# Performance work log

Measured on AMD Instinct MI355X. Metric: run time of the kernel, lower is better.

## Reference

```python
import jax, jax.numpy as jnp
import numpy as np

B, L, E, H, EXP = 2, 2048, 1024, 16, 4
D = E // H
EPS = 1e-5

def layernorm(x, g, b):
    mu = jnp.mean(x, axis=-1, keepdims=True)
    var = jnp.var(x, axis=-1, keepdims=True)
    return (x - mu) * jax.lax.rsqrt(var + EPS) * g + b

def setup_inputs() -> dict:
    key = jax.random.key(0)
    ks = jax.random.split(key, 12)
    s = 0.02
    return {
        "x": jax.random.normal(ks[0], (B, L, E), dtype=jnp.float32),
        "ln1_g": jnp.ones((E,), jnp.float32),
        "ln1_b": jnp.zeros((E,), jnp.float32),
        "W_qkv": jax.random.normal(ks[1], (E, 3 * E), dtype=jnp.float32) * s,
        "W_proj": jax.random.normal(ks[2], (E, E), dtype=jnp.float32) * s,
        "b_proj": jnp.zeros((E,), jnp.float32),
        "ln2_g": jnp.ones((E,), jnp.float32),
        "ln2_b": jnp.zeros((E,), jnp.float32),
        "W1": jax.random.normal(ks[3], (E, EXP * E), dtype=jnp.float32) * s,
        "b1": jnp.zeros((EXP * E,), jnp.float32),
        "W2": jax.random.normal(ks[4], (EXP * E, E), dtype=jnp.float32) * s,
        "b2": jnp.zeros((E,), jnp.float32),
    }

def reference(x, ln1_g, ln1_b, W_qkv, W_proj, b_proj, ln2_g, ln2_b, W1, b1, W2, b2):
    # --- attention sub-block (pre-LN) ---
    h = layernorm(x, ln1_g, ln1_b)                      # [B,L,E]
    qkv = h @ W_qkv                                      # [B,L,3E]
    q, k, v = jnp.split(qkv, 3, axis=-1)
    q = q.reshape(B, L, H, D).transpose(0, 2, 1, 3)      # [B,H,L,D]
    k = k.reshape(B, L, H, D).transpose(0, 2, 1, 3)
    v = v.reshape(B, L, H, D).transpose(0, 2, 1, 3)
    scale = jnp.sqrt(jnp.float32(E))                     # NOTE: module divides by sqrt(E), not sqrt(D)
    att = jnp.einsum('bhqd,bhkd->bhqk', q, k) / scale
    att = jax.nn.softmax(att, axis=-1)
    out = jnp.einsum('bhqk,bhkd->bhqd', att, v)          # [B,H,L,D]
    out = out.transpose(0, 2, 1, 3).reshape(B, L, E)
    x = x + out @ W_proj + b_proj                         # residual
    # --- feed-forward sub-block (pre-LN) ---
    h = layernorm(x, ln2_g, ln2_b)
    h = jax.nn.gelu(h @ W1 + b1, approximate=False)       # torch GELU is exact erf
    x = x + h @ W2 + b2
    return x
```

## Files before the change

kernel.cpp:

```cpp
#include <hip/hip_runtime.h>
#include <cstdint>
#include <cstddef>


typedef __bf16 bht;
typedef __attribute__((ext_vector_type(8))) __bf16 bf16x8;
typedef __attribute__((ext_vector_type(4))) __bf16 bf16x4;
typedef __attribute__((ext_vector_type(4))) float f32x4;
typedef __attribute__((ext_vector_type(4))) short short4v;

#define B_ 2
#define L_ 2048
#define E_ 1024
#define H_ 16
#define D_ 64
#define ROWS_ (B_ * L_)

#define QSCALE_ 0.045084441f

__device__ __forceinline__ void glds16(const void* g, void* l) {
    __builtin_amdgcn_global_load_lds(
        (const __attribute__((address_space(1))) unsigned int*)g,
        (__attribute__((address_space(3))) unsigned int*)l, 16, 0, 0);
}

__device__ __forceinline__ short4v as_s4(bf16x4 v) {
    return __builtin_bit_cast(short4v, v);
}

__device__ __forceinline__ float fast_exp2(float x) {
#if __has_builtin(__builtin_amdgcn_exp2f)
    return __builtin_amdgcn_exp2f(x);
#else
    return exp2f(x);
#endif
}

__global__ __launch_bounds__(256)
void transpose_cast(const float* __restrict__ in, bht* __restrict__ out, int R, int C) {
    __shared__ float tile[32][33];
    const int bx = blockIdx.x * 32;
    const int by = blockIdx.y * 32;
    const int tx = threadIdx.x, ty = threadIdx.y;
    #pragma unroll
    for (int i = 0; i < 32; i += 8)
        tile[ty + i][tx] = in[(size_t)(by + ty + i) * C + bx + tx];
    __syncthreads();
    #pragma unroll
    for (int i = 0; i < 32; i += 8)
        out[(size_t)(bx + ty + i) * R + by + tx] = (bht)tile[tx][ty + i];
}

__global__ __launch_bounds__(256)
void ln_kernel(const float* __restrict__ x, const float* __restrict__ g,
               const float* __restrict__ b, bht* __restrict__ out) {
    const int row = blockIdx.x, t = threadIdx.x;
    const float4 v = ((const float4*)(x + (size_t)row * E_))[t];
    float s  = v.x + v.y + v.z + v.w;
    float ss = v.x*v.x + v.y*v.y + v.z*v.z + v.w*v.w;
    #pragma unroll
    for (int off = 32; off > 0; off >>= 1) {
        s  += __shfl_down(s, off);
        ss += __shfl_down(ss, off);
    }
    __shared__ float red[8];
    const int wave = t >> 6, lane = t & 63;
    if (lane == 0) { red[wave] = s; red[4 + wave] = ss; }
    __syncthreads();
    s  = red[0] + red[1] + red[2] + red[3];
    ss = red[4] + red[5] + red[6] + red[7];
    const float mean = s * (1.0f / (float)E_);
    const float var  = ss * (1.0f / (float)E_) - mean * mean;
    const float rstd = rsqrtf(var + 1e-5f);
    const float4 gv = ((const float4*)g)[t];
    const float4 bv = ((const float4*)b)[t];
    bf16x4 o;
    o.x = (bht)((v.x - mean) * rstd * gv.x + bv.x);
    o.y = (bht)((v.y - mean) * rstd * gv.y + bv.y);
    o.z = (bht)((v.z - mean) * rstd * gv.z + bv.z);
    o.w = (bht)((v.w - mean) * rstd * gv.w + bv.w);
    *(bf16x4*)(out + (size_t)row * E_ + t * 4) = o;
}

enum { EPI_QKV = 0, EPI_RESID = 1, EPI_GELU = 2 };

template <int EPI>
__global__ __launch_bounds__(512, 2)
void gemm256(const bht* __restrict__ A, const bht* __restrict__ Bt,
             const float* __restrict__ bias, void* __restrict__ outp,
             bht* __restrict__ qo, bht* __restrict__ ko, bht* __restrict__ vto,
             int M, int N, int K) {
    __shared__ __align__(16) char smem_[98304];
    const int t = threadIdx.x;
    const int lane = t & 63, wave = t >> 6;
    const int lane15 = lane & 15, quad = lane >> 4;
    const int waveM = wave >> 2, waveN = wave & 3;
    const int bm = blockIdx.y * 256, bn = blockIdx.x * 256;

    f32x4 acc[8][4];
    #pragma unroll
    for (int i = 0; i < 8; ++i)
        #pragma unroll
        for (int j = 0; j < 4; ++j)
            acc[i][j] = f32x4{0.f, 0.f, 0.f, 0.f};

    const int apc = ((quad ^ (lane15 & 3)) & 3) * 8;
    const int aoff = waveM * 4096 + lane15 * 32 + apc;
    const int boff = waveN * 2048 + lane15 * 32 + apc;

    auto stage_step = [&](int s, int op, int bufi) {
        const int k0 = s * 32;
        const bht* src = op ? Bt : A;
        const int rb = op ? bn : bm;
        char* dst = smem_ + (size_t)bufi * 32768 + op * 16384;
        #pragma unroll
        for (int i = 0; i < 2; ++i) {
            const int g = i * 512 + t;
            const int row = g >> 2;
            const int c = ((g & 3) ^ (row & 3)) * 8;
            glds16(src + (size_t)(rb + row) * K + k0 + c, dst + (size_t)g * 16);
        }
    };

    const int NT = K >> 5;
    stage_step(0, 0, 0); stage_step(0, 1, 0);
    stage_step(1, 0, 1); stage_step(1, 1, 1);

    int cb = 0;
    for (int s = 0; s < NT; ++s) {
        const int nb2 = (cb >= 1) ? cb - 1 : 2;
        if (s + 2 < NT) {
            stage_step(s + 2, 0, nb2);
            asm volatile("s_waitcnt vmcnt(6)" ::: "memory");
        } else if (s + 1 < NT) {
            asm volatile("s_waitcnt vmcnt(4)" ::: "memory");
        } else {
            asm volatile("s_waitcnt vmcnt(0)" ::: "memory");
        }
        __builtin_amdgcn_s_barrier();
        asm volatile("" ::: "memory");

        const bht* Au = (const bht*)(smem_ + (size_t)cb * 32768);
        const bht* Bu = (const bht*)(smem_ + (size_t)cb * 32768 + 16384);
        bf16x8 af0[4], bfv[4];
        #pragma unroll
        for (int m = 0; m < 4; ++m)
            af0[m] = *(const bf16x8*)(Au + aoff + m * 512);
        #pragma unroll
        for (int n = 0; n < 4; ++n)
            bfv[n] = *(const bf16x8*)(Bu + boff + n * 512);
        asm volatile("s_waitcnt lgkmcnt(0)" ::: "memory");
        __builtin_amdgcn_s_setprio(1);
        #pragma unroll
        for (int m = 0; m < 4; ++m)
            #pragma unroll
            for (int n = 0; n < 4; ++n)
                acc[m][n] = __builtin_amdgcn_mfma_f32_16x16x32_bf16(af0[m], bfv[n], acc[m][n], 0, 0, 0);
        __builtin_amdgcn_s_setprio(0);
        __builtin_amdgcn_s_barrier();
        asm volatile("" ::: "memory");

        bf16x8 af1[4];
        #pragma unroll
        for (int m = 0; m < 4; ++m)
            af1[m] = *(const bf16x8*)(Au + aoff + (m + 4) * 512);
        if (s + 2 < NT) stage_step(s + 2, 1, nb2);
        asm volatile("s_waitcnt lgkmcnt(0)" ::: "memory");
        __builtin_amdgcn_s_setprio(1);
        #pragma unroll
        for (int m = 0; m < 4; ++m)
            #pragma unroll
            for (int n = 0; n < 4; ++n)
                acc[m + 4][n] = __builtin_amdgcn_mfma_f32_16x16x32_bf16(af1[m], bfv[n], acc[m + 4][n], 0, 0, 0);
        __builtin_amdgcn_s_setprio(0);
        __builtin_amdgcn_s_barrier();
        asm volatile("" ::: "memory");

        cb = (cb == 2) ? 0 : cb + 1;
    }

    if constexpr (EPI == EPI_GELU) {
        #pragma unroll
        for (int m = 0; m < 8; ++m) {
            const int row0 = bm + waveM * 128 + m * 16 + quad * 4;
            #pragma unroll
            for (int n = 0; n < 4; ++n) {
                const int col = bn + waveN * 64 + n * 16 + lane15;
                #pragma unroll
                for (int r = 0; r < 4; ++r) {
                    float v = acc[m][n][r] + bias[col];
                    v = 0.5f * v * (1.0f + erff(v * 0.70710678118654752f));
                    ((bht*)outp)[(size_t)(row0 + r) * N + col] = (bht)v;
                }
            }
        }
    } else {
        const int b = bm >> 11, l0 = bm & 2047;
        if (bn >= 2048) {
            bht* Vtile = (bht*)smem_;
            #pragma unroll
            for (int h = 0; h < 2; ++h) {
                if ((waveN >> 1) == h) {
                    #pragma unroll
                    for (int m = 0; m < 8; ++m) {
                        const int rl0 = waveM * 128 + m * 16 + quad * 4;
                        #pragma unroll
                        for (int n = 0; n < 4; ++n) {
                            const int c = (waveN & 1) * 64 + n * 16 + lane15;
                            #pragma unroll
                            for (int r = 0; r < 4; ++r)
                                Vtile[(size_t)c * 264 + rl0 + r] = (bht)acc[m][n][r];
                        }
                    }
                }
                __syncthreads();
                #pragma unroll
                for (int it = 0; it < 4; ++it) {
                    const int c2 = it * 32 + (t >> 4);
                    const int cg = (bn - 2048) + h * 128 + c2;
                    const int hh = cg >> 6, d = cg & 63;
                    const int bh2 = b * H_ + hh;
                    #pragma unroll
                    for (int half2 = 0; half2 < 2; ++half2) {
                        const int ch = (t & 15) + 16 * half2;
                        bf16x8 vv = *(const bf16x8*)(Vtile + (size_t)c2 * 264 + ch * 8);
                        if (d & 8)
                            vv = __builtin_shufflevector(vv, vv, 4, 5, 6, 7, 0, 1, 2, 3);
                        *(bf16x8*)(vto + ((size_t)bh2 * D_ + d) * L_ + l0 + ch * 8) = vv;
                    }
                }
                __syncthreads();
            }
        } else {
            #pragma unroll
            for (int m = 0; m < 8; ++m) {
                const int row0 = bm + waveM * 128 + m * 16 + quad * 4;
                #pragma unroll
                for (int n = 0; n < 4; ++n) {
                    const int col = bn + waveN * 64 + n * 16 + lane15;
                    const int seg = col >> 10;
                    const int c = col & 1023;
                    const int hh = c >> 6, d = c & 63;
                    #pragma unroll
                    for (int r = 0; r < 4; ++r) {
                        const int mrow = row0 + r;
                        const int bb = mrow >> 11, l = mrow & 2047;
                        const int bh2 = bb * H_ + hh;
                        const float v = acc[m][n][r];
                        if (seg == 0)
                            qo[((size_t)bh2 * L_ + l) * D_ + d] = (bht)(v * QSCALE_);
                        else
                            ko[((size_t)bh2 * L_ + l) * D_ + d] = (bht)v;
                    }
                }
            }
        }
    }
    (void)M;
}

template <int EPI>
__global__ __launch_bounds__(256)
void gemm_bt64(const bht* __restrict__ A, const bht* __restrict__ Bt,
               const float* __restrict__ bias, const float* __restrict__ resid,
               void* __restrict__ outp, int M, int N, int K) {
    __shared__ __align__(16) bht As[64 * 64];
    __shared__ __align__(16) bht Bs[128 * 64];
    const int t = threadIdx.x;
    const int lane = t & 63, wave = t >> 6;
    const int lane15 = lane & 15, quad = lane >> 4;
    const int waveM = wave >> 1, waveN = wave & 1;
    const int bm = blockIdx.y * 64, bn = blockIdx.x * 128;

    f32x4 acc[2][4];
    #pragma unroll
    for (int i = 0; i < 2; ++i)
        #pragma unroll
        for (int j = 0; j < 4; ++j)
            acc[i][j] = f32x4{0.f, 0.f, 0.f, 0.f};

    const int swz = lane15 & 7;

    for (int k0 = 0; k0 < K; k0 += 64) {
        #pragma unroll
        for (int i = 0; i < 2; ++i) {
            const int g = i * 256 + t;
            const int row = g >> 3;
            const int col = ((g & 7) ^ (row & 7)) * 8;
            glds16(A + (size_t)(bm + row) * K + k0 + col, (char*)As + (size_t)g * 16);
        }
        #pragma unroll
        for (int i = 0; i < 4; ++i) {
            const int g = i * 256 + t;
            const int row = g >> 3;
            const int col = ((g & 7) ^ (row & 7)) * 8;
            glds16(Bt + (size_t)(bn + row) * K + k0 + col, (char*)Bs + (size_t)g * 16);
        }
        __syncthreads();
        #pragma unroll
        for (int kk = 0; kk < 2; ++kk) {
            const int pc = ((kk * 4 + quad) ^ swz) * 8;
            bf16x8 af[2], bfv[4];
            #pragma unroll
            for (int i = 0; i < 2; ++i)
                af[i] = *(const bf16x8*)(As + (waveM * 32 + i * 16 + lane15) * 64 + pc);
            #pragma unroll
            for (int j = 0; j < 4; ++j)
                bfv[j] = *(const bf16x8*)(Bs + (waveN * 64 + j * 16 + lane15) * 64 + pc);
            #pragma unroll
            for (int i = 0; i < 2; ++i)
                #pragma unroll
                for (int j = 0; j < 4; ++j)
                    acc[i][j] = __builtin_amdgcn_mfma_f32_16x16x32_bf16(af[i], bfv[j], acc[i][j], 0, 0, 0);
        }
        __syncthreads();
    }

    #pragma unroll
    for (int i = 0; i < 2; ++i) {
        const int row0 = bm + waveM * 32 + i * 16 + quad * 4;
        #pragma unroll
        for (int j = 0; j < 4; ++j) {
            const int col = bn + waveN * 64 + j * 16 + lane15;
            #pragma unroll
            for (int r = 0; r < 4; ++r) {
                const int m = row0 + r;
                float v = acc[i][j][r];
                if (EPI == EPI_RESID) {
                    ((float*)outp)[(size_t)m * N + col] =
                        v + bias[col] + resid[(size_t)m * N + col];
                } else {
                    v += bias[col];
                    v = 0.5f * v * (1.0f + erff(v * 0.70710678118654752f));
                    ((bht*)outp)[(size_t)m * N + col] = (bht)v;
                }
            }
        }
    }
}

#define KT_ 128
#define NT_ (L_ / KT_)

__global__ __launch_bounds__(256)
void attn_kernel(const bht* __restrict__ Q, const bht* __restrict__ Kb,
                 const bht* __restrict__ Vt, bht* __restrict__ O) {
    __shared__ __align__(16) bht Ks[KT_ * 64];
    __shared__ __align__(16) bht Vs[64 * KT_];
    __shared__ float Ls[4][16];
    const int t = threadIdx.x;
    const int lane = t & 63, wave = t >> 6;
    const int lane15 = lane & 15, quad = lane >> 4;
    const int bh = blockIdx.x, qt = blockIdx.y;

    const bht* Qh = Q  + (size_t)bh * L_ * D_;
    const bht* Kh = Kb + (size_t)bh * L_ * D_;
    const bht* Vh = Vt + (size_t)bh * D_ * L_;

    const int q0 = qt * 64 + wave * 16;

    bf16x8 aq[2];
    #pragma unroll
    for (int kc = 0; kc < 2; ++kc)
        aq[kc] = *(const bf16x8*)(Qh + (size_t)(q0 + lane15) * D_ + kc * 32 + quad * 8);

    f32x4 o_acc[4];
    #pragma unroll
    for (int db = 0; db < 4; ++db) o_acc[db] = f32x4{0.f, 0.f, 0.f, 0.f};
    float l_sum = 0.f;

    const int pc0 = (quad ^ (lane15 & 7)) * 8;
    const int pc1 = pc0 ^ 32;
    const int vhalf4 = ((quad & 1) ^ ((lane15 >> 3) & 1)) * 4;

    auto stageK = [&](int kt2) {
        const int key0 = kt2 * KT_;
        #pragma unroll
        for (int i = 0; i < 4; ++i) {
            const int g = i * 256 + t;
            const int krow = g >> 3;
            const int ksc = ((g & 7) ^ (krow & 7)) * 8;
            glds16(Kh + (size_t)(key0 + krow) * D_ + ksc, (char*)Ks + (size_t)g * 16);
        }
    };
    auto stageV = [&](int kt2) {
        const int key0 = kt2 * KT_;
        #pragma unroll
        for (int i = 0; i < 4; ++i) {
            const int g = i * 256 + t;
            const int vrow = g >> 4;
            const int vsc = ((g & 15) ^ (vrow & 7)) * 8;
            glds16(Vh + (size_t)vrow * L_ + key0 + vsc, (char*)Vs + (size_t)g * 16);
        }
    };

    stageK(0);
    stageV(0);

    for (int kt = 0; kt < NT_; ++kt) {
        asm volatile("s_waitcnt vmcnt(4) lgkmcnt(0)" ::: "memory");
        __builtin_amdgcn_s_barrier();

        __builtin_amdgcn_s_setprio(1);
        short4v pk[8];
        #pragma unroll
        for (int nb = 0; nb < 8; ++nb) {
            const bf16x8 ak0 = *(const bf16x8*)(Ks + (nb * 16 + lane15) * 64 + pc0);
            const bf16x8 ak1 = *(const bf16x8*)(Ks + (nb * 16 + lane15) * 64 + pc1);
            f32x4 st = __builtin_amdgcn_mfma_f32_16x16x32_bf16(
                ak0, aq[0], f32x4{0.f, 0.f, 0.f, 0.f}, 0, 0, 0);
            st = __builtin_amdgcn_mfma_f32_16x16x32_bf16(ak1, aq[1], st, 0, 0, 0);
            bf16x4 pkv;
            #pragma unroll
            for (int r = 0; r < 4; ++r) {
                const float pv = fast_exp2(st[r]);
                l_sum += pv;
                pkv[r] = (bht)pv;
            }
            pk[nb] = as_s4(pkv);
        }
        __builtin_amdgcn_s_setprio(0);

        asm volatile("s_waitcnt vmcnt(0) lgkmcnt(0)" ::: "memory");
        __builtin_amdgcn_s_barrier();
        if (kt + 1 < NT_) stageK(kt + 1);

        __builtin_amdgcn_s_setprio(1);
        #pragma unroll
        for (int nb = 0; nb < 8; ++nb) {
            #pragma unroll
            for (int db = 0; db < 4; ++db) {
                const int row = db * 16 + lane15;
                const int c16 = (nb * 2 + (quad >> 1)) ^ (row & 7);
                const bf16x4 bv = *(const bf16x4*)(Vs + row * KT_ + c16 * 8 + vhalf4);
                o_acc[db] = __builtin_amdgcn_mfma_f32_16x16x16bf16_1k(
                    pk[nb], as_s4(bv), o_acc[db], 0, 0, 0);
            }
        }
        __builtin_amdgcn_s_setprio(0);

        asm volatile("s_waitcnt lgkmcnt(0)" ::: "memory");
        __builtin_amdgcn_s_barrier();
        if (kt + 1 < NT_) stageV(kt + 1);
    }

    l_sum += __shfl_xor(l_sum, 16);
    l_sum += __shfl_xor(l_sum, 32);
    Ls[wave][lane15] = l_sum;
    asm volatile("s_waitcnt lgkmcnt(0)" ::: "memory");

    const int b = bh >> 4, h = bh & 15;
    #pragma unroll
    for (int r = 0; r < 4; ++r) {
        const int l = q0 + quad * 4 + r;
        const float inv = 1.0f / Ls[wave][quad * 4 + r];
        #pragma unroll
        for (int db = 0; db < 4; ++db)
            O[((size_t)b * L_ + l) * E_ + h * 64 + db * 16 + lane15] =
                (bht)(o_acc[db][r] * inv);
    }
}

extern "C" void kernel_launch(void* const* d_in, const int* in_sizes, int n_in,
                              void* d_out, int out_size, void* d_ws, size_t ws_size,
                              hipStream_t stream) {
    const float* x      = (const float*)d_in[0];
    const float* ln1_g  = (const float*)d_in[1];
    const float* ln1_b  = (const float*)d_in[2];
    const float* W_qkv  = (const float*)d_in[3];
    const float* W_proj = (const float*)d_in[4];
    const float* b_proj = (const float*)d_in[5];
    const float* ln2_g  = (const float*)d_in[6];
    const float* ln2_b  = (const float*)d_in[7];
    const float* W1     = (const float*)d_in[8];
    const float* b1     = (const float*)d_in[9];
    const float* W2     = (const float*)d_in[10];
    const float* b2     = (const float*)d_in[11];
    float* out = (float*)d_out;

    char* ws = (char*)d_ws;
    auto alloc = [&](size_t bytes) {
        char* p = ws;
        ws += (bytes + 255) & ~(size_t)255;
        return p;
    };
    bht*   WqkvT  = (bht*)alloc((size_t)3072 * 1024 * 2);
    bht*   WprojT = (bht*)alloc((size_t)1024 * 1024 * 2);
    bht*   W1T    = (bht*)alloc((size_t)4096 * 1024 * 2);
    bht*   W2T    = (bht*)alloc((size_t)1024 * 4096 * 2);
    bht*   hb     = (bht*)alloc((size_t)ROWS_ * E_ * 2);
    float* x1     = (float*)alloc((size_t)ROWS_ * E_ * 4);
    bht*   Qb     = (bht*)alloc((size_t)B_ * H_ * L_ * D_ * 2);
    bht*   Kbuf   = (bht*)alloc((size_t)B_ * H_ * L_ * D_ * 2);
    bht*   Vtb    = (bht*)alloc((size_t)B_ * H_ * D_ * L_ * 2);
    bht*   attno  = (bht*)alloc((size_t)ROWS_ * E_ * 2);
    bht*   ffn1   = Qb;

    transpose_cast<<<dim3(3072 / 32, 1024 / 32), dim3(32, 8), 0, stream>>>(W_qkv, WqkvT, 1024, 3072);
    transpose_cast<<<dim3(1024 / 32, 1024 / 32), dim3(32, 8), 0, stream>>>(W_proj, WprojT, 1024, 1024);
    transpose_cast<<<dim3(4096 / 32, 1024 / 32), dim3(32, 8), 0, stream>>>(W1, W1T, 1024, 4096);
    transpose_cast<<<dim3(1024 / 32, 4096 / 32), dim3(32, 8), 0, stream>>>(W2, W2T, 4096, 1024);

    ln_kernel<<<ROWS_, 256, 0, stream>>>(x, ln1_g, ln1_b, hb);

    gemm256<EPI_QKV><<<dim3(3072 / 256, ROWS_ / 256), 512, 0, stream>>>(
        hb, WqkvT, nullptr, nullptr, Qb, Kbuf, Vtb, ROWS_, 3072, 1024);

    attn_kernel<<<dim3(B_ * H_, L_ / 64), 256, 0, stream>>>(Qb, Kbuf, Vtb, attno);

    gemm_bt64<EPI_RESID><<<dim3(1024 / 128, ROWS_ / 64), 256, 0, stream>>>(
        attno, WprojT, b_proj, x, x1, ROWS_, 1024, 1024);

    ln_kernel<<<ROWS_, 256, 0, stream>>>(x1, ln2_g, ln2_b, hb);

    gemm256<EPI_GELU><<<dim3(4096 / 256, ROWS_ / 256), 512, 0, stream>>>(
        hb, W1T, b1, ffn1, nullptr, nullptr, nullptr, ROWS_, 4096, 1024);

    gemm_bt64<EPI_RESID><<<dim3(1024 / 128, ROWS_ / 64), 256, 0, stream>>>(
        ffn1, W2T, b2, x1, out, ROWS_, 1024, 4096);

    (void)in_sizes; (void)n_in; (void)out_size; (void)ws_size;
}
```

Baseline: 354.7 us.

## Double-buffer LDS in the 64x128 GEMM and remap blocks per XCD

Turns the projection and FFN2 GEMM kernel into a two-stage pipeline: the next K tile is issued as an async global-to-LDS load while the current tile is consumed, with explicit vmcnt waits and raw barriers in place of __syncthreads. It also remaps block indices so each XCD works on a contiguous band of M rows, to improve L2 reuse, and raises wave priority around the MFMA section. The goal is to hide global load latency behind the matrix math. The cost is twice the LDS (48KB), which may lower occupancy, and the vmcnt(6) count has to match exactly the number of loads issued per stage.

```diff
diff --git a/kernel.cpp b/kernel.cpp
--- a/kernel.cpp
+++ b/kernel.cpp
@@ -261,16 +261,20 @@
 
 template <int EPI>
 __global__ __launch_bounds__(256)
-void gemm_bt64(const bht* __restrict__ A, const bht* __restrict__ Bt,
-               const float* __restrict__ bias, const float* __restrict__ resid,
-               void* __restrict__ outp, int M, int N, int K) {
-    __shared__ __align__(16) bht As[64 * 64];
-    __shared__ __align__(16) bht Bs[128 * 64];
+void gemm_pipe64(const bht* __restrict__ A, const bht* __restrict__ Bt,
+                 const float* __restrict__ bias, const float* __restrict__ resid,
+                 void* __restrict__ outp, int M, int N, int K) {
+    __shared__ __align__(16) char smem_[49152];
     const int t = threadIdx.x;
     const int lane = t & 63, wave = t >> 6;
     const int lane15 = lane & 15, quad = lane >> 4;
     const int waveM = wave >> 1, waveN = wave & 1;
-    const int bm = blockIdx.y * 64, bn = blockIdx.x * 128;
+
+    const int flat = blockIdx.y * gridDim.x + blockIdx.x;
+    const int xcd = flat & 7;
+    const int w = flat >> 3;
+    const int bm = (xcd * (gridDim.y >> 3) + (w >> 3)) * 64;
+    const int bn = (w & 7) * 128;
 
     f32x4 acc[2][4];
     #pragma unroll
@@ -281,22 +285,40 @@
 
     const int swz = lane15 & 7;
 
-    for (int k0 = 0; k0 < K; k0 += 64) {
+    auto stage = [&](int s, int bufi) {
+        const int k0 = s * 64;
+        char* base = smem_ + (size_t)bufi * 24576;
         #pragma unroll
         for (int i = 0; i < 2; ++i) {
             const int g = i * 256 + t;
             const int row = g >> 3;
             const int col = ((g & 7) ^ (row & 7)) * 8;
-            glds16(A + (size_t)(bm + row) * K + k0 + col, (char*)As + (size_t)g * 16);
+            glds16(A + (size_t)(bm + row) * K + k0 + col, base + (size_t)g * 16);
         }
         #pragma unroll
         for (int i = 0; i < 4; ++i) {
             const int g = i * 256 + t;
             const int row = g >> 3;
             const int col = ((g & 7) ^ (row & 7)) * 8;
-            glds16(Bt + (size_t)(bn + row) * K + k0 + col, (char*)Bs + (size_t)g * 16);
-        }
-        __syncthreads();
+            glds16(Bt + (size_t)(bn + row) * K + k0 + col, base + 8192 + (size_t)g * 16);
+        }
+    };
+
+    const int NT = K >> 6;
+    stage(0, 0);
+    for (int s = 0; s < NT; ++s) {
+        if (s + 1 < NT) {
+            stage(s + 1, (s + 1) & 1);
+            asm volatile("s_waitcnt vmcnt(6)" ::: "memory");
+        } else {
+            asm volatile("s_waitcnt vmcnt(0)" ::: "memory");
+        }
+        __builtin_amdgcn_s_barrier();
+        asm volatile("" ::: "memory");
+
+        const bht* As = (const bht*)(smem_ + (size_t)(s & 1) * 24576);
+        const bht* Bs = (const bht*)(smem_ + (size_t)(s & 1) * 24576 + 8192);
+        __builtin_amdgcn_s_setprio(1);
         #pragma unroll
         for (int kk = 0; kk < 2; ++kk) {
             const int pc = ((kk * 4 + quad) ^ swz) * 8;
@@ -313,7 +335,10 @@
                 for (int j = 0; j < 4; ++j)
                     acc[i][j] = __builtin_amdgcn_mfma_f32_16x16x32_bf16(af[i], bfv[j], acc[i][j], 0, 0, 0);
         }
-        __syncthreads();
+        __builtin_amdgcn_s_setprio(0);
+        asm volatile("s_waitcnt lgkmcnt(0)" ::: "memory");
+        __builtin_amdgcn_s_barrier();
+        asm volatile("" ::: "memory");
     }
 
     #pragma unroll
@@ -508,7 +533,7 @@
 
     attn_kernel<<<dim3(B_ * H_, L_ / 64), 256, 0, stream>>>(Qb, Kbuf, Vtb, attno);
 
-    gemm_bt64<EPI_RESID><<<dim3(1024 / 128, ROWS_ / 64), 256, 0, stream>>>(
+    gemm_pipe64<EPI_RESID><<<dim3(1024 / 128, ROWS_ / 64), 256, 0, stream>>>(
         attno, WprojT, b_proj, x, x1, ROWS_, 1024, 1024);
 
     ln_kernel<<<ROWS_, 256, 0, stream>>>(x1, ln2_g, ln2_b, hb);
@@ -516,7 +541,7 @@
     gemm256<EPI_GELU><<<dim3(4096 / 256, ROWS_ / 256), 512, 0, stream>>>(
         hb, W1T, b1, ffn1, nullptr, nullptr, nullptr, ROWS_, 4096, 1024);
 
-    gemm_bt64<EPI_RESID><<<dim3(1024 / 128, ROWS_ / 64), 256, 0, stream>>>(
+    gemm_pipe64<EPI_RESID><<<dim3(1024 / 128, ROWS_ / 64), 256, 0, stream>>>(
         ffn1, W2T, b2, x1, out, ROWS_, 1024, 4096);
 
     (void)in_sizes; (void)n_in; (void)out_size; (void)ws_size;
```

Result: faster. 332.1 us (-6.4%).
